# Kernel tuning notes

Hardware: AMD Instinct MI355X
Metric: run time of the kernel (lower is better)

The kernel has to match this reference:

```python
import jax, jax.numpy as jnp
import numpy as np

N, M = 50000, 2048          # nodes, observations
E, O = 512, 256             # in_features_embed, in_features_obs
EPS = 1e-6


def setup_inputs() -> dict:
    key = jax.random.key(0)
    k1, k2, k3, k4, k5 = jax.random.split(key, 5)
    scale_e = 1.0 / np.sqrt(E)
    scale_o = 1.0 / np.sqrt(O)
    return {
        "node_feature": jax.random.normal(k1, (N, E), dtype=jnp.float32),
        "obs_feature": jax.random.normal(k2, (M, O), dtype=jnp.float32),
        # nn.Linear weights, stored as [out, in] like torch
        "W_q": jax.random.normal(k3, (E, E), dtype=jnp.float32) * scale_e,
        "W_k": jax.random.normal(k4, (E, O), dtype=jnp.float32) * scale_o,
        "W_v": jax.random.normal(k5, (E, O), dtype=jnp.float32) * scale_o,
        "ln_gamma": jnp.ones((E,), dtype=jnp.float32),
        "ln_beta": jnp.zeros((E,), dtype=jnp.float32),
    }


def layer_norm(x, gamma, beta, eps=EPS):
    mu = jnp.mean(x, axis=-1, keepdims=True)
    var = jnp.mean(jnp.square(x - mu), axis=-1, keepdims=True)
    return (x - mu) * jax.lax.rsqrt(var + eps) * gamma + beta


def reference(node_feature, obs_feature, W_q, W_k, W_v, ln_gamma, ln_beta):
    # projections (torch Linear: x @ W.T)
    q = node_feature @ W_q.T            # [N, E]
    k = obs_feature @ W_k.T             # [M, E]
    v = obs_feature @ W_v.T             # [M, E]
    # un-normalized cross-attention (no softmax), original association
    attn = q @ k.T                      # [N, M]
    out = attn @ v                      # [N, E]
    return layer_norm(out + node_feature, ln_gamma, ln_beta)
```

## Files before the change

### kernel.cpp

```cpp
#include <hip/hip_runtime.h>
#include <hip/hip_bf16.h>

#define NROWS 50000
#define MOBS  2048
#define EDIM  512
#define ODIM  256
#define BM2   128
#define NT2   391

typedef short s16x8 __attribute__((ext_vector_type(8)));
typedef float f32x4 __attribute__((ext_vector_type(4)));

typedef const __attribute__((address_space(1))) unsigned int* gptr_t;
typedef __attribute__((address_space(3))) unsigned int* lptr_t;

__device__ __forceinline__ unsigned short f32_to_bf16(float f) {
    unsigned int u = __float_as_uint(f);
    u += 0x7fffu + ((u >> 16) & 1u);
    return (unsigned short)(u >> 16);
}

__device__ __forceinline__ s16x8 pack8(f32x4 a, f32x4 b) {
    unsigned int p0, p1, p2, p3;
    asm("v_cvt_pk_bf16_f32 %0, %1, %2" : "=v"(p0) : "v"(a[0]), "v"(a[1]));
    asm("v_cvt_pk_bf16_f32 %0, %1, %2" : "=v"(p1) : "v"(a[2]), "v"(a[3]));
    asm("v_cvt_pk_bf16_f32 %0, %1, %2" : "=v"(p2) : "v"(b[0]), "v"(b[1]));
    asm("v_cvt_pk_bf16_f32 %0, %1, %2" : "=v"(p3) : "v"(b[2]), "v"(b[3]));
    union { unsigned int u[4]; s16x8 v; } r;
    r.u[0] = p0; r.u[1] = p1; r.u[2] = p2; r.u[3] = p3;
    return r.v;
}

__global__ __launch_bounds__(256) void gp_fused(const float* __restrict__ obs,
                                                const float* __restrict__ Wq,
                                                const float* __restrict__ Wk,
                                                float* __restrict__ G,
                                                float* __restrict__ P) {
    __shared__ float SA[16][68];
    __shared__ float SB[16][68];
    const int b = blockIdx.x;
    const float *A, *B;
    float* C;
    int lda, ldb, k_lo, k_hi, bx, by;
    if (b < 256) {
        bx = b & 3; by = (b >> 2) & 3; int bz = b >> 4;
        A = obs; B = obs; C = G; lda = ODIM; ldb = ODIM;
        k_lo = bz * (MOBS / 16); k_hi = k_lo + MOBS / 16;
    } else {
        int i = b - 256;
        bx = i & 3; by = (i >> 2) & 7; int bz = i >> 5;
        A = Wq; B = Wk; C = P; lda = EDIM; ldb = ODIM;
        k_lo = bz * (EDIM / 4); k_hi = k_lo + EDIM / 4;
    }
    const int t  = threadIdx.x;
    const int tx = t & 15, ty = t >> 4;
    const int i0 = by * 64, j0 = bx * 64;

    float acc[4][4];
#pragma unroll
    for (int a = 0; a < 4; ++a)
#pragma unroll
        for (int c2 = 0; c2 < 4; ++c2) acc[a][c2] = 0.f;

    for (int k0 = k_lo; k0 < k_hi; k0 += 16) {
#pragma unroll
        for (int r = 0; r < 4; ++r) {
            int idx = t + 256 * r;
            int mm = idx & 63, kk2 = idx >> 6;
            SA[kk2][mm] = A[(size_t)(k0 + kk2) * lda + i0 + mm];
        }
#pragma unroll
        for (int r = 0; r < 4; ++r) {
            int idx = t + 256 * r;
            int jj = idx & 63, kk2 = idx >> 6;
            SB[kk2][jj] = B[(size_t)(k0 + kk2) * ldb + j0 + jj];
        }
        __syncthreads();
#pragma unroll
        for (int kk2 = 0; kk2 < 16; ++kk2) {
            float4 a4 = *(const float4*)&SA[kk2][ty * 4];
            float4 b4 = *(const float4*)&SB[kk2][tx * 4];
            float av[4] = {a4.x, a4.y, a4.z, a4.w};
            float bv[4] = {b4.x, b4.y, b4.z, b4.w};
#pragma unroll
            for (int a = 0; a < 4; ++a)
#pragma unroll
                for (int c2 = 0; c2 < 4; ++c2) acc[a][c2] += av[a] * bv[c2];
        }
        __syncthreads();
    }
#pragma unroll
    for (int a = 0; a < 4; ++a)
#pragma unroll
        for (int c2 = 0; c2 < 4; ++c2)
            atomicAdd(&C[(size_t)(i0 + ty * 4 + a) * ODIM + j0 + tx * 4 + c2],
                      acc[a][c2]);
}

template <int TA, int TB, int SPLIT, int FRAG>
__global__ __launch_bounds__(256) void sgemm4(const float* __restrict__ A,
                                              const float* __restrict__ B,
                                              void* __restrict__ Cv,
                                              int NN, int KK, int lda, int ldb) {
    __shared__ float SA[16][68];
    __shared__ float SB[16][68];
    const int t  = threadIdx.x;
    const int tx = t & 15, ty = t >> 4;
    const int i0 = blockIdx.y * 64, j0 = blockIdx.x * 64;
    int k_lo = 0, k_hi = KK;
    if (SPLIT > 1) { int ch = KK / SPLIT; k_lo = blockIdx.z * ch; k_hi = k_lo + ch; }

    float acc[4][4];
#pragma unroll
    for (int a = 0; a < 4; ++a)
#pragma unroll
        for (int b = 0; b < 4; ++b) acc[a][b] = 0.f;

    for (int k0 = k_lo; k0 < k_hi; k0 += 16) {
#pragma unroll
        for (int r = 0; r < 4; ++r) {
            int idx = t + 256 * r;
            int mm, kk2;
            if (TA) { mm = idx & 63; kk2 = idx >> 6; }
            else    { kk2 = idx & 15; mm = idx >> 4; }
            SA[kk2][mm] = TA ? A[(size_t)(k0 + kk2) * lda + i0 + mm]
                             : A[(size_t)(i0 + mm) * lda + k0 + kk2];
        }
#pragma unroll
        for (int r = 0; r < 4; ++r) {
            int idx = t + 256 * r;
            int jj, kk2;
            if (TB) { kk2 = idx & 15; jj = idx >> 4; }
            else    { jj = idx & 63; kk2 = idx >> 6; }
            SB[kk2][jj] = TB ? B[(size_t)(j0 + jj) * ldb + k0 + kk2]
                             : B[(size_t)(k0 + kk2) * ldb + j0 + jj];
        }
        __syncthreads();
#pragma unroll
        for (int kk2 = 0; kk2 < 16; ++kk2) {
            float4 a4 = *(const float4*)&SA[kk2][ty * 4];
            float4 b4 = *(const float4*)&SB[kk2][tx * 4];
            float av[4] = {a4.x, a4.y, a4.z, a4.w};
            float bv[4] = {b4.x, b4.y, b4.z, b4.w};
#pragma unroll
            for (int a = 0; a < 4; ++a)
#pragma unroll
                for (int b = 0; b < 4; ++b) acc[a][b] += av[a] * bv[b];
        }
        __syncthreads();
    }

    if (FRAG) {
        unsigned short* C = (unsigned short*)Cv;
#pragma unroll
        for (int a = 0; a < 4; ++a)
#pragma unroll
            for (int b = 0; b < 4; ++b) {
                int i = i0 + ty * 4 + a;
                int j = j0 + tx * 4 + b;
                float v = acc[a][b] + (i == j ? 1.f : 0.f);
                size_t idx = ((size_t)(((i >> 5) * 32 + (j >> 4)) * 64
                               + ((i >> 3) & 3) * 16 + (j & 15))) * 8 + (i & 7);
                C[idx] = f32_to_bf16(v);
            }
    } else if (SPLIT > 1) {
        float* C = (float*)Cv;
#pragma unroll
        for (int a = 0; a < 4; ++a)
#pragma unroll
            for (int b = 0; b < 4; ++b)
                atomicAdd(&C[(size_t)(i0 + ty * 4 + a) * NN + j0 + tx * 4 + b],
                          acc[a][b]);
    } else {
        float* C = (float*)Cv;
#pragma unroll
        for (int a = 0; a < 4; ++a) {
            float4 o = make_float4(acc[a][0], acc[a][1], acc[a][2], acc[a][3]);
            *(float4*)&C[(size_t)(i0 + ty * 4 + a) * NN + j0 + tx * 4] = o;
        }
    }
}

__global__ __launch_bounds__(512, 2) void gemm_m97_ln(
    const float* __restrict__ node, const unsigned short* __restrict__ Uf,
    const float* __restrict__ gamma, const float* __restrict__ beta,
    float* __restrict__ out) {
    __shared__ char smem[98304];
    float* Ab = (float*)smem;
    char*  Bb = smem + 32768;
    float* lds_s  = (float*)smem;
    float* lds_q  = (float*)smem + 512;
    float* lds_mu = (float*)smem + 1024;
    float* lds_rs = (float*)smem + 1152;

    const int t  = threadIdx.x;
    const int w  = t >> 6, l = t & 63;
    const int rg = w >> 2, cg = w & 3;
    const int lr = l & 15, lk = l >> 4;
    const int m0 = blockIdx.x * BM2;

    const int sr = w * 8 + (l >> 3);
    const int schunk = (l & 7) ^ ((l >> 3) & 7);
    int gr0 = m0 + sr;      if (gr0 > NROWS - 1) gr0 = NROWS - 1;
    int gr1 = m0 + sr + 64; if (gr1 > NROWS - 1) gr1 = NROWS - 1;
    const char* asrc0 = (const char*)node + (size_t)gr0 * 2048 + schunk * 16;
    const char* asrc1 = (const char*)node + (size_t)gr1 * 2048 + schunk * 16;
    const char* bsrc  = (const char*)Uf + (size_t)w * 4096 + (size_t)l * 16;

    auto dma = [&](int buf, int kt) {
        char* ad = (char*)(Ab + buf * 4096) + w * 1024;
        __builtin_amdgcn_global_load_lds((gptr_t)(asrc0 + kt * 128),
                                         (lptr_t)ad, 16, 0, 0);
        __builtin_amdgcn_global_load_lds((gptr_t)(asrc1 + kt * 128),
                                         (lptr_t)(ad + 8192), 16, 0, 0);
        char* bd = Bb + buf * 32768 + w * 4096;
        const char* bs = bsrc + (size_t)kt * 32768;
#pragma unroll
        for (int j = 0; j < 4; ++j)
            __builtin_amdgcn_global_load_lds((gptr_t)(bs + j * 1024),
                                             (lptr_t)(bd + j * 1024), 16, 0, 0);
    };

    f32x4 acc[4][8];
#pragma unroll
    for (int mi = 0; mi < 4; ++mi)
#pragma unroll
        for (int ni = 0; ni < 8; ++ni)
            acc[mi][ni] = (f32x4){0.f, 0.f, 0.f, 0.f};

    dma(0, 0);
    __syncthreads();

#pragma unroll 1
    for (int kt = 0; kt < 16; ++kt) {
        if (kt < 15) dma((kt + 1) & 1, kt + 1);

        const int cur = kt & 1;
        const char* bbase = Bb + cur * 32768 + cg * 8192 + l * 16;
        s16x8 bfr[8];
#pragma unroll
        for (int ni = 0; ni < 8; ++ni)
            bfr[ni] = *(const s16x8*)(bbase + ni * 1024);

        s16x8 afr[4];
#pragma unroll
        for (int mi = 0; mi < 4; ++mi) {
            int row = rg * 64 + mi * 16 + lr;
            const char* rb = (const char*)(Ab + cur * 4096) + row * 128;
            f32x4 a0 = *(const f32x4*)(rb + ((2 * lk)     ^ (lr & 7)) * 16);
            f32x4 a1 = *(const f32x4*)(rb + ((2 * lk + 1) ^ (lr & 7)) * 16);
            afr[mi] = pack8(a0, a1);
        }
#pragma unroll
        for (int mi = 0; mi < 4; ++mi)
#pragma unroll
            for (int ni = 0; ni < 8; ++ni)
                acc[mi][ni] = __builtin_amdgcn_mfma_f32_16x16x32_bf16(
                    afr[mi], bfr[ni], acc[mi][ni], 0, 0, 0);

        __syncthreads();
    }

#pragma unroll
    for (int mi = 0; mi < 4; ++mi) {
#pragma unroll
        for (int j = 0; j < 4; ++j) {
            float sm = 0.f, q = 0.f;
#pragma unroll
            for (int ni = 0; ni < 8; ++ni) {
                float v = acc[mi][ni][j];
                sm += v; q += v * v;
            }
#pragma unroll
            for (int off = 1; off < 16; off <<= 1) {
                sm += __shfl_xor(sm, off);
                q  += __shfl_xor(q, off);
            }
            if (lr == 0) {
                int row = rg * 64 + mi * 16 + lk * 4 + j;
                lds_s[cg * 128 + row] = sm;
                lds_q[cg * 128 + row] = q;
            }
        }
    }
    __syncthreads();
    if (t < 128) {
        float sm = lds_s[t] + lds_s[128 + t] + lds_s[256 + t] + lds_s[384 + t];
        float q  = lds_q[t] + lds_q[128 + t] + lds_q[256 + t] + lds_q[384 + t];
        float mu  = sm * (1.f / (float)EDIM);
        float var = q * (1.f / (float)EDIM) - mu * mu;
        lds_mu[t] = mu;
        lds_rs[t] = rsqrtf(var + 1e-6f);
    }
    __syncthreads();

    float gv[8], bv[8];
#pragma unroll
    for (int ni = 0; ni < 8; ++ni) {
        int col = cg * 128 + ni * 16 + lr;
        gv[ni] = gamma[col];
        bv[ni] = beta[col];
    }

#pragma unroll
    for (int mi = 0; mi < 4; ++mi) {
#pragma unroll
        for (int j = 0; j < 4; ++j) {
            int row = rg * 64 + mi * 16 + lk * 4 + j;
            int gr = m0 + row;
            if (gr < NROWS) {
                float mu = lds_mu[row], rs = lds_rs[row];
                float* op = out + (size_t)gr * EDIM + cg * 128 + lr;
#pragma unroll
                for (int ni = 0; ni < 8; ++ni)
                    op[ni * 16] = (acc[mi][ni][j] - mu) * rs * gv[ni] + bv[ni];
            }
        }
    }
}

extern "C" void kernel_launch(void* const* d_in, const int* in_sizes, int n_in,
                              void* d_out, int out_size, void* d_ws, size_t ws_size,
                              hipStream_t stream) {
    const float* node  = (const float*)d_in[0];
    const float* obs   = (const float*)d_in[1];
    const float* Wq    = (const float*)d_in[2];
    const float* Wk    = (const float*)d_in[3];
    const float* Wv    = (const float*)d_in[4];
    const float* gamma = (const float*)d_in[5];
    const float* beta  = (const float*)d_in[6];
    float* out = (float*)d_out;

    float* ws = (float*)d_ws;
    float*          G  = ws;
    float*          P  = G  + ODIM * ODIM;
    float*          PG = P  + EDIM * ODIM;
    unsigned short* Uf = (unsigned short*)(PG + EDIM * ODIM);

    hipMemsetAsync((void*)G, 0,
                   (ODIM * ODIM + 2 * EDIM * ODIM) * sizeof(float), stream);

    gp_fused<<<dim3(384), 256, 0, stream>>>(obs, Wq, Wk, G, P);
    sgemm4<0, 0, 2, 0><<<dim3(4, 8, 2), 256, 0, stream>>>(P, G, PG, ODIM, ODIM, ODIM, ODIM);
    sgemm4<0, 1, 1, 1><<<dim3(8, 8, 1), 256, 0, stream>>>(PG, Wv, Uf, EDIM, ODIM, ODIM, ODIM);
    gemm_m97_ln<<<dim3(NT2), 512, 0, stream>>>(node, Uf, gamma, beta, out);
}
```

Measured before the change: 125.4 us.

## Fuse small precompute GEMM chain with grid barriers; triple-buffer main GEMM

```diff
diff --git a/kernel.cpp b/kernel.cpp
--- a/kernel.cpp
+++ b/kernel.cpp
@@ -31,163 +31,187 @@
     return r.v;
 }
 
-__global__ __launch_bounds__(256) void gp_fused(const float* __restrict__ obs,
-                                                const float* __restrict__ Wq,
-                                                const float* __restrict__ Wk,
-                                                float* __restrict__ G,
-                                                float* __restrict__ P) {
+__device__ __forceinline__ void gridbar(unsigned int* c, unsigned int nb) {
+    __syncthreads();
+    if (threadIdx.x == 0) {
+        __hip_atomic_fetch_add(c, 1u, __ATOMIC_ACQ_REL, __HIP_MEMORY_SCOPE_AGENT);
+        while (__hip_atomic_load(c, __ATOMIC_ACQUIRE, __HIP_MEMORY_SCOPE_AGENT) < nb)
+            __builtin_amdgcn_s_sleep(8);
+    }
+    __syncthreads();
+}
+
+__global__ __launch_bounds__(256) void chain_fused(
+    const float* __restrict__ obs, const float* __restrict__ Wq,
+    const float* __restrict__ Wk, const float* __restrict__ Wv,
+    float* __restrict__ G, float* __restrict__ P, float* __restrict__ PG,
+    unsigned short* __restrict__ Uf, unsigned int* __restrict__ bar) {
     __shared__ float SA[16][68];
     __shared__ float SB[16][68];
     const int b = blockIdx.x;
-    const float *A, *B;
-    float* C;
-    int lda, ldb, k_lo, k_hi, bx, by;
-    if (b < 256) {
-        bx = b & 3; by = (b >> 2) & 3; int bz = b >> 4;
-        A = obs; B = obs; C = G; lda = ODIM; ldb = ODIM;
-        k_lo = bz * (MOBS / 16); k_hi = k_lo + MOBS / 16;
-    } else {
-        int i = b - 256;
-        bx = i & 3; by = (i >> 2) & 7; int bz = i >> 5;
-        A = Wq; B = Wk; C = P; lda = EDIM; ldb = ODIM;
-        k_lo = bz * (EDIM / 4); k_hi = k_lo + EDIM / 4;
-    }
-    const int t  = threadIdx.x;
+    const int t = threadIdx.x;
     const int tx = t & 15, ty = t >> 4;
-    const int i0 = by * 64, j0 = bx * 64;
-
-    float acc[4][4];
-#pragma unroll
-    for (int a = 0; a < 4; ++a)
-#pragma unroll
-        for (int c2 = 0; c2 < 4; ++c2) acc[a][c2] = 0.f;
-
-    for (int k0 = k_lo; k0 < k_hi; k0 += 16) {
-#pragma unroll
-        for (int r = 0; r < 4; ++r) {
-            int idx = t + 256 * r;
-            int mm = idx & 63, kk2 = idx >> 6;
-            SA[kk2][mm] = A[(size_t)(k0 + kk2) * lda + i0 + mm];
-        }
-#pragma unroll
-        for (int r = 0; r < 4; ++r) {
-            int idx = t + 256 * r;
-            int jj = idx & 63, kk2 = idx >> 6;
-            SB[kk2][jj] = B[(size_t)(k0 + kk2) * ldb + j0 + jj];
-        }
-        __syncthreads();
-#pragma unroll
-        for (int kk2 = 0; kk2 < 16; ++kk2) {
-            float4 a4 = *(const float4*)&SA[kk2][ty * 4];
-            float4 b4 = *(const float4*)&SB[kk2][tx * 4];
-            float av[4] = {a4.x, a4.y, a4.z, a4.w};
-            float bv[4] = {b4.x, b4.y, b4.z, b4.w};
-#pragma unroll
-            for (int a = 0; a < 4; ++a)
-#pragma unroll
-                for (int c2 = 0; c2 < 4; ++c2) acc[a][c2] += av[a] * bv[c2];
-        }
-        __syncthreads();
-    }
-#pragma unroll
-    for (int a = 0; a < 4; ++a)
-#pragma unroll
-        for (int c2 = 0; c2 < 4; ++c2)
-            atomicAdd(&C[(size_t)(i0 + ty * 4 + a) * ODIM + j0 + tx * 4 + c2],
-                      acc[a][c2]);
-}
-
-template <int TA, int TB, int SPLIT, int FRAG>
-__global__ __launch_bounds__(256) void sgemm4(const float* __restrict__ A,
-                                              const float* __restrict__ B,
-                                              void* __restrict__ Cv,
-                                              int NN, int KK, int lda, int ldb) {
-    __shared__ float SA[16][68];
-    __shared__ float SB[16][68];
-    const int t  = threadIdx.x;
-    const int tx = t & 15, ty = t >> 4;
-    const int i0 = blockIdx.y * 64, j0 = blockIdx.x * 64;
-    int k_lo = 0, k_hi = KK;
-    if (SPLIT > 1) { int ch = KK / SPLIT; k_lo = blockIdx.z * ch; k_hi = k_lo + ch; }
-
-    float acc[4][4];
-#pragma unroll
-    for (int a = 0; a < 4; ++a)
-#pragma unroll
-        for (int b = 0; b < 4; ++b) acc[a][b] = 0.f;
-
-    for (int k0 = k_lo; k0 < k_hi; k0 += 16) {
-#pragma unroll
-        for (int r = 0; r < 4; ++r) {
-            int idx = t + 256 * r;
-            int mm, kk2;
-            if (TA) { mm = idx & 63; kk2 = idx >> 6; }
-            else    { kk2 = idx & 15; mm = idx >> 4; }
-            SA[kk2][mm] = TA ? A[(size_t)(k0 + kk2) * lda + i0 + mm]
-                             : A[(size_t)(i0 + mm) * lda + k0 + kk2];
-        }
-#pragma unroll
-        for (int r = 0; r < 4; ++r) {
-            int idx = t + 256 * r;
-            int jj, kk2;
-            if (TB) { kk2 = idx & 15; jj = idx >> 4; }
-            else    { jj = idx & 63; kk2 = idx >> 6; }
-            SB[kk2][jj] = TB ? B[(size_t)(j0 + jj) * ldb + k0 + kk2]
-                             : B[(size_t)(k0 + kk2) * ldb + j0 + jj];
-        }
-        __syncthreads();
-#pragma unroll
-        for (int kk2 = 0; kk2 < 16; ++kk2) {
-            float4 a4 = *(const float4*)&SA[kk2][ty * 4];
-            float4 b4 = *(const float4*)&SB[kk2][tx * 4];
-            float av[4] = {a4.x, a4.y, a4.z, a4.w};
-            float bv[4] = {b4.x, b4.y, b4.z, b4.w};
-#pragma unroll
-            for (int a = 0; a < 4; ++a)
-#pragma unroll
-                for (int b = 0; b < 4; ++b) acc[a][b] += av[a] * bv[b];
-        }
-        __syncthreads();
-    }
-
-    if (FRAG) {
-        unsigned short* C = (unsigned short*)Cv;
-#pragma unroll
-        for (int a = 0; a < 4; ++a)
-#pragma unroll
-            for (int b = 0; b < 4; ++b) {
+
+    {
+        size_t base = (size_t)b * 256 + t;
+        G[base] = 0.f;
+        G[base + 98304] = 0.f;
+    }
+    gridbar(bar + 0, 384);
+
+    {
+        const float *A, *B;
+        float* C;
+        int lda, ldb, k_lo, k_hi, bx, by;
+        if (b < 256) {
+            bx = b & 3; by = (b >> 2) & 3; int bz = b >> 4;
+            A = obs; B = obs; C = G; lda = ODIM; ldb = ODIM;
+            k_lo = bz * (MOBS / 16); k_hi = k_lo + MOBS / 16;
+        } else {
+            int i = b - 256;
+            bx = i & 3; by = (i >> 2) & 7; int bz = i >> 5;
+            A = Wq; B = Wk; C = P; lda = EDIM; ldb = ODIM;
+            k_lo = bz * (EDIM / 4); k_hi = k_lo + EDIM / 4;
+        }
+        const int i0 = by * 64, j0 = bx * 64;
+        float acc[4][4];
+#pragma unroll
+        for (int a = 0; a < 4; ++a)
+#pragma unroll
+            for (int c2 = 0; c2 < 4; ++c2) acc[a][c2] = 0.f;
+        for (int k0 = k_lo; k0 < k_hi; k0 += 16) {
+#pragma unroll
+            for (int r = 0; r < 4; ++r) {
+                int idx = t + 256 * r;
+                int mm = idx & 63, kk2 = idx >> 6;
+                SA[kk2][mm] = A[(size_t)(k0 + kk2) * lda + i0 + mm];
+            }
+#pragma unroll
+            for (int r = 0; r < 4; ++r) {
+                int idx = t + 256 * r;
+                int jj = idx & 63, kk2 = idx >> 6;
+                SB[kk2][jj] = B[(size_t)(k0 + kk2) * ldb + j0 + jj];
+            }
+            __syncthreads();
+#pragma unroll
+            for (int kk2 = 0; kk2 < 16; ++kk2) {
+                float4 a4 = *(const float4*)&SA[kk2][ty * 4];
+                float4 b4 = *(const float4*)&SB[kk2][tx * 4];
+                float av[4] = {a4.x, a4.y, a4.z, a4.w};
+                float bv[4] = {b4.x, b4.y, b4.z, b4.w};
+#pragma unroll
+                for (int a = 0; a < 4; ++a)
+#pragma unroll
+                    for (int c2 = 0; c2 < 4; ++c2) acc[a][c2] += av[a] * bv[c2];
+            }
+            __syncthreads();
+        }
+#pragma unroll
+        for (int a = 0; a < 4; ++a)
+#pragma unroll
+            for (int c2 = 0; c2 < 4; ++c2)
+                atomicAdd(&C[(size_t)(i0 + ty * 4 + a) * ODIM + j0 + tx * 4 + c2],
+                          acc[a][c2]);
+    }
+    gridbar(bar + 1, 384);
+
+    if (b < 32) {
+        const int i0 = (b >> 2) * 64, j0 = (b & 3) * 64;
+        float acc[4][4];
+#pragma unroll
+        for (int a = 0; a < 4; ++a)
+#pragma unroll
+            for (int c2 = 0; c2 < 4; ++c2) acc[a][c2] = 0.f;
+        for (int k0 = 0; k0 < ODIM; k0 += 16) {
+#pragma unroll
+            for (int r = 0; r < 4; ++r) {
+                int idx = t + 256 * r;
+                int kk2 = idx & 15, mm = idx >> 4;
+                SA[kk2][mm] = P[(size_t)(i0 + mm) * ODIM + k0 + kk2];
+            }
+#pragma unroll
+            for (int r = 0; r < 4; ++r) {
+                int idx = t + 256 * r;
+                int jj = idx & 63, kk2 = idx >> 6;
+                SB[kk2][jj] = G[(size_t)(k0 + kk2) * ODIM + j0 + jj];
+            }
+            __syncthreads();
+#pragma unroll
+            for (int kk2 = 0; kk2 < 16; ++kk2) {
+                float4 a4 = *(const float4*)&SA[kk2][ty * 4];
+                float4 b4 = *(const float4*)&SB[kk2][tx * 4];
+                float av[4] = {a4.x, a4.y, a4.z, a4.w};
+                float bv[4] = {b4.x, b4.y, b4.z, b4.w};
+#pragma unroll
+                for (int a = 0; a < 4; ++a)
+#pragma unroll
+                    for (int c2 = 0; c2 < 4; ++c2) acc[a][c2] += av[a] * bv[c2];
+            }
+            __syncthreads();
+        }
+#pragma unroll
+        for (int a = 0; a < 4; ++a) {
+            float4 o = make_float4(acc[a][0], acc[a][1], acc[a][2], acc[a][3]);
+            *(float4*)&PG[(size_t)(i0 + ty * 4 + a) * ODIM + j0 + tx * 4] = o;
+        }
+    }
+    gridbar(bar + 2, 384);
+
+    if (b < 64) {
+        const int i0 = (b >> 3) * 64, j0 = (b & 7) * 64;
+        float acc[4][4];
+#pragma unroll
+        for (int a = 0; a < 4; ++a)
+#pragma unroll
+            for (int c2 = 0; c2 < 4; ++c2) acc[a][c2] = 0.f;
+        for (int k0 = 0; k0 < ODIM; k0 += 16) {
+#pragma unroll
+            for (int r = 0; r < 4; ++r) {
+                int idx = t + 256 * r;
+                int kk2 = idx & 15, mm = idx >> 4;
+                SA[kk2][mm] = PG[(size_t)(i0 + mm) * ODIM + k0 + kk2];
+            }
+#pragma unroll
+            for (int r = 0; r < 4; ++r) {
+                int idx = t + 256 * r;
+                int kk2 = idx & 15, jj = idx >> 4;
+                SB[kk2][jj] = Wv[(size_t)(j0 + jj) * ODIM + k0 + kk2];
+            }
+            __syncthreads();
+#pragma unroll
+            for (int kk2 = 0; kk2 < 16; ++kk2) {
+                float4 a4 = *(const float4*)&SA[kk2][ty * 4];
+                float4 b4 = *(const float4*)&SB[kk2][tx * 4];
+                float av[4] = {a4.x, a4.y, a4.z, a4.w};
+                float bv[4] = {b4.x, b4.y, b4.z, b4.w};
+#pragma unroll
+                for (int a = 0; a < 4; ++a)
+#pragma unroll
+                    for (int c2 = 0; c2 < 4; ++c2) acc[a][c2] += av[a] * bv[c2];
+            }
+            __syncthreads();
+        }
+#pragma unroll
+        for (int a = 0; a < 4; ++a)
+#pragma unroll
+            for (int c2 = 0; c2 < 4; ++c2) {
                 int i = i0 + ty * 4 + a;
-                int j = j0 + tx * 4 + b;
-                float v = acc[a][b] + (i == j ? 1.f : 0.f);
+                int j = j0 + tx * 4 + c2;
+                float v = acc[a][c2] + (i == j ? 1.f : 0.f);
                 size_t idx = ((size_t)(((i >> 5) * 32 + (j >> 4)) * 64
                                + ((i >> 3) & 3) * 16 + (j & 15))) * 8 + (i & 7);
-                C[idx] = f32_to_bf16(v);
-            }
-    } else if (SPLIT > 1) {
-        float* C = (float*)Cv;
-#pragma unroll
-        for (int a = 0; a < 4; ++a)
-#pragma unroll
-            for (int b = 0; b < 4; ++b)
-                atomicAdd(&C[(size_t)(i0 + ty * 4 + a) * NN + j0 + tx * 4 + b],
-                          acc[a][b]);
-    } else {
-        float* C = (float*)Cv;
-#pragma unroll
-        for (int a = 0; a < 4; ++a) {
-            float4 o = make_float4(acc[a][0], acc[a][1], acc[a][2], acc[a][3]);
-            *(float4*)&C[(size_t)(i0 + ty * 4 + a) * NN + j0 + tx * 4] = o;
-        }
-    }
-}
-
-__global__ __launch_bounds__(512, 2) void gemm_m97_ln(
+                Uf[idx] = f32_to_bf16(v);
+            }
+    }
+}
+
+__global__ __launch_bounds__(512, 2) void gemm_pipe_ln(
     const float* __restrict__ node, const unsigned short* __restrict__ Uf,
     const float* __restrict__ gamma, const float* __restrict__ beta,
     float* __restrict__ out) {
-    __shared__ char smem[98304];
-    float* Ab = (float*)smem;
-    char*  Bb = smem + 32768;
+    __shared__ char smem[147456];
+    char* Areg = smem;
+    char* Breg = smem + 49152;
     float* lds_s  = (float*)smem;
     float* lds_q  = (float*)smem + 512;
     float* lds_mu = (float*)smem + 1024;
@@ -208,12 +232,12 @@
     const char* bsrc  = (const char*)Uf + (size_t)w * 4096 + (size_t)l * 16;
 
     auto dma = [&](int buf, int kt) {
-        char* ad = (char*)(Ab + buf * 4096) + w * 1024;
+        char* ad = Areg + buf * 16384 + w * 1024;
         __builtin_amdgcn_global_load_lds((gptr_t)(asrc0 + kt * 128),
                                          (lptr_t)ad, 16, 0, 0);
         __builtin_amdgcn_global_load_lds((gptr_t)(asrc1 + kt * 128),
                                          (lptr_t)(ad + 8192), 16, 0, 0);
-        char* bd = Bb + buf * 32768 + w * 4096;
+        char* bd = Breg + buf * 32768 + w * 4096;
         const char* bs = bsrc + (size_t)kt * 32768;
 #pragma unroll
         for (int j = 0; j < 4; ++j)
@@ -228,25 +252,17 @@
         for (int ni = 0; ni < 8; ++ni)
             acc[mi][ni] = (f32x4){0.f, 0.f, 0.f, 0.f};
 
-    dma(0, 0);
-    __syncthreads();
-
-#pragma unroll 1
-    for (int kt = 0; kt < 16; ++kt) {
-        if (kt < 15) dma((kt + 1) & 1, kt + 1);
-
-        const int cur = kt & 1;
-        const char* bbase = Bb + cur * 32768 + cg * 8192 + l * 16;
+    auto compute = [&](int cur) {
+        const char* bbase = Breg + cur * 32768 + cg * 8192 + l * 16;
         s16x8 bfr[8];
 #pragma unroll
         for (int ni = 0; ni < 8; ++ni)
             bfr[ni] = *(const s16x8*)(bbase + ni * 1024);
-
         s16x8 afr[4];
 #pragma unroll
         for (int mi = 0; mi < 4; ++mi) {
             int row = rg * 64 + mi * 16 + lr;
-            const char* rb = (const char*)(Ab + cur * 4096) + row * 128;
+            const char* rb = Areg + cur * 16384 + row * 128;
             f32x4 a0 = *(const f32x4*)(rb + ((2 * lk)     ^ (lr & 7)) * 16);
             f32x4 a1 = *(const f32x4*)(rb + ((2 * lk + 1) ^ (lr & 7)) * 16);
             afr[mi] = pack8(a0, a1);
@@ -257,9 +273,30 @@
             for (int ni = 0; ni < 8; ++ni)
                 acc[mi][ni] = __builtin_amdgcn_mfma_f32_16x16x32_bf16(
                     afr[mi], bfr[ni], acc[mi][ni], 0, 0, 0);
-
-        __syncthreads();
-    }
+    };
+
+    dma(0, 0);
+    dma(1, 1);
+
+#pragma unroll 1
+    for (int kt = 0; kt < 14; ++kt) {
+        dma((kt + 2) % 3, kt + 2);
+        asm volatile("s_waitcnt vmcnt(12)" ::: "memory");
+        __builtin_amdgcn_sched_barrier(0);
+        __builtin_amdgcn_s_barrier();
+        compute(kt % 3);
+        __builtin_amdgcn_s_barrier();
+    }
+    asm volatile("s_waitcnt vmcnt(6)" ::: "memory");
+    __builtin_amdgcn_sched_barrier(0);
+    __builtin_amdgcn_s_barrier();
+    compute(14 % 3);
+    __builtin_amdgcn_s_barrier();
+    asm volatile("s_waitcnt vmcnt(0)" ::: "memory");
+    __builtin_amdgcn_sched_barrier(0);
+    __builtin_amdgcn_s_barrier();
+    compute(15 % 3);
+    __syncthreads();
 
 #pragma unroll
     for (int mi = 0; mi < 4; ++mi) {
@@ -336,12 +373,9 @@
     float*          P  = G  + ODIM * ODIM;
     float*          PG = P  + EDIM * ODIM;
     unsigned short* Uf = (unsigned short*)(PG + EDIM * ODIM);
-
-    hipMemsetAsync((void*)G, 0,
-                   (ODIM * ODIM + 2 * EDIM * ODIM) * sizeof(float), stream);
-
-    gp_fused<<<dim3(384), 256, 0, stream>>>(obs, Wq, Wk, G, P);
-    sgemm4<0, 0, 2, 0><<<dim3(4, 8, 2), 256, 0, stream>>>(P, G, PG, ODIM, ODIM, ODIM, ODIM);
-    sgemm4<0, 1, 1, 1><<<dim3(8, 8, 1), 256, 0, stream>>>(PG, Wv, Uf, EDIM, ODIM, ODIM, ODIM);
-    gemm_m97_ln<<<dim3(NT2), 512, 0, stream>>>(node, Uf, gamma, beta, out);
-}
+    unsigned int*   bar = (unsigned int*)((char*)d_ws + (8u << 20));
+
+    hipMemsetAsync((void*)bar, 0, 64, stream);
+    chain_fused<<<dim3(384), 256, 0, stream>>>(obs, Wq, Wk, Wv, G, P, PG, Uf, bar);
+    gemm_pipe_ln<<<dim3(NT2), 512, 0, stream>>>(node, Uf, gamma, beta, out);
+}
```

After: 241.0 us. 92.2% more time.

## Triple-buffer LDS loads with explicit vmcnt waits in final GEMM+LayerNorm kernel

Applied to the files above, without the earlier changes.

```diff
diff --git a/kernel.cpp b/kernel.cpp
--- a/kernel.cpp
+++ b/kernel.cpp
@@ -181,13 +181,13 @@
     }
 }
 
-__global__ __launch_bounds__(512, 2) void gemm_m97_ln(
+__global__ __launch_bounds__(512, 2) void gemm_pipe_ln(
     const float* __restrict__ node, const unsigned short* __restrict__ Uf,
     const float* __restrict__ gamma, const float* __restrict__ beta,
     float* __restrict__ out) {
-    __shared__ char smem[98304];
-    float* Ab = (float*)smem;
-    char*  Bb = smem + 32768;
+    __shared__ char smem[147456];
+    char* Areg = smem;
+    char* Breg = smem + 49152;
     float* lds_s  = (float*)smem;
     float* lds_q  = (float*)smem + 512;
     float* lds_mu = (float*)smem + 1024;
@@ -208,12 +208,12 @@
     const char* bsrc  = (const char*)Uf + (size_t)w * 4096 + (size_t)l * 16;
 
     auto dma = [&](int buf, int kt) {
-        char* ad = (char*)(Ab + buf * 4096) + w * 1024;
+        char* ad = Areg + buf * 16384 + w * 1024;
         __builtin_amdgcn_global_load_lds((gptr_t)(asrc0 + kt * 128),
                                          (lptr_t)ad, 16, 0, 0);
         __builtin_amdgcn_global_load_lds((gptr_t)(asrc1 + kt * 128),
                                          (lptr_t)(ad + 8192), 16, 0, 0);
-        char* bd = Bb + buf * 32768 + w * 4096;
+        char* bd = Breg + buf * 32768 + w * 4096;
         const char* bs = bsrc + (size_t)kt * 32768;
 #pragma unroll
         for (int j = 0; j < 4; ++j)
@@ -228,25 +228,17 @@
         for (int ni = 0; ni < 8; ++ni)
             acc[mi][ni] = (f32x4){0.f, 0.f, 0.f, 0.f};
 
-    dma(0, 0);
-    __syncthreads();
-
-#pragma unroll 1
-    for (int kt = 0; kt < 16; ++kt) {
-        if (kt < 15) dma((kt + 1) & 1, kt + 1);
-
-        const int cur = kt & 1;
-        const char* bbase = Bb + cur * 32768 + cg * 8192 + l * 16;
+    auto compute = [&](int cur) {
+        const char* bbase = Breg + cur * 32768 + cg * 8192 + l * 16;
         s16x8 bfr[8];
 #pragma unroll
         for (int ni = 0; ni < 8; ++ni)
             bfr[ni] = *(const s16x8*)(bbase + ni * 1024);
-
         s16x8 afr[4];
 #pragma unroll
         for (int mi = 0; mi < 4; ++mi) {
             int row = rg * 64 + mi * 16 + lr;
-            const char* rb = (const char*)(Ab + cur * 4096) + row * 128;
+            const char* rb = Areg + cur * 16384 + row * 128;
             f32x4 a0 = *(const f32x4*)(rb + ((2 * lk)     ^ (lr & 7)) * 16);
             f32x4 a1 = *(const f32x4*)(rb + ((2 * lk + 1) ^ (lr & 7)) * 16);
             afr[mi] = pack8(a0, a1);
@@ -257,9 +249,30 @@
             for (int ni = 0; ni < 8; ++ni)
                 acc[mi][ni] = __builtin_amdgcn_mfma_f32_16x16x32_bf16(
                     afr[mi], bfr[ni], acc[mi][ni], 0, 0, 0);
-
-        __syncthreads();
-    }
+    };
+
+    dma(0, 0);
+    dma(1, 1);
+
+#pragma unroll 1
+    for (int kt = 0; kt < 14; ++kt) {
+        dma((kt + 2) % 3, kt + 2);
+        asm volatile("s_waitcnt vmcnt(12)" ::: "memory");
+        __builtin_amdgcn_sched_barrier(0);
+        __builtin_amdgcn_s_barrier();
+        compute(kt % 3);
+        __builtin_amdgcn_s_barrier();
+    }
+    asm volatile("s_waitcnt vmcnt(6)" ::: "memory");
+    __builtin_amdgcn_sched_barrier(0);
+    __builtin_amdgcn_s_barrier();
+    compute(14 % 3);
+    __builtin_amdgcn_s_barrier();
+    asm volatile("s_waitcnt vmcnt(0)" ::: "memory");
+    __builtin_amdgcn_sched_barrier(0);
+    __builtin_amdgcn_s_barrier();
+    compute(15 % 3);
+    __syncthreads();
 
 #pragma unroll
     for (int mi = 0; mi < 4; ++mi) {
@@ -343,5 +356,5 @@
     gp_fused<<<dim3(384), 256, 0, stream>>>(obs, Wq, Wk, G, P);
     sgemm4<0, 0, 2, 0><<<dim3(4, 8, 2), 256, 0, stream>>>(P, G, PG, ODIM, ODIM, ODIM, ODIM);
     sgemm4<0, 1, 1, 1><<<dim3(8, 8, 1), 256, 0, stream>>>(PG, Wv, Uf, EDIM, ODIM, ODIM, ODIM);
-    gemm_m97_ln<<<dim3(NT2), 512, 0, stream>>>(node, Uf, gamma, beta, out);
-}
+    gemm_pipe_ln<<<dim3(NT2), 512, 0, stream>>>(node, Uf, gamma, beta, out);
+}
```

Measured after the change: 125.0 us. No clear change (-0.3%).
